# Performance work log

Hardware: AMD Instinct MI355X
Metric: run time of the kernel (lower is better)

Reference implementation:

```python
import jax, jax.numpy as jnp
import numpy as np

D = 512
B = 128
V = 1024
MAX_LEN = 5000


def _pos_encoding(d, max_len):
    # sinusoidal PE table [max_len, d], identical to the torch buffer
    pos = np.arange(max_len, dtype=np.float32)[:, None]
    div = np.exp(np.arange(0, d, 2, dtype=np.float32) * (-np.log(10000.0) / d))
    pe = np.zeros((max_len, d), dtype=np.float32)
    pe[:, 0::2] = np.sin(pos * div)
    pe[:, 1::2] = np.cos(pos * div)
    return jnp.asarray(pe)


def setup_inputs() -> dict:
    key = jax.random.key(0)
    ks = jax.random.split(key, 16)
    s = 0.02  # weight scale
    return {
        "x": jax.random.normal(ks[0], (B, V), jnp.float32),
        "timesteps": jax.random.randint(ks[1], (B,), 0, 1000),
        "query_emb": jax.random.normal(ks[2], (B, D), jnp.float32),
        "target_emb": jax.random.normal(ks[3], (B, V, D), jnp.float32),
        "Wq": jax.random.normal(ks[4], (D, D), jnp.float32) * s,
        "Wk": jax.random.normal(ks[5], (D, D), jnp.float32) * s,
        "Wv": jax.random.normal(ks[6], (D, D), jnp.float32) * s,
        "Wp": jax.random.normal(ks[7], (D, D), jnp.float32) * s,
        "bp": jnp.zeros((D,), jnp.float32),
        "Wt1": jax.random.normal(ks[8], (D, D), jnp.float32) * s,
        "bt1": jnp.zeros((D,), jnp.float32),
        "Wt2": jax.random.normal(ks[9], (D, D), jnp.float32) * s,
        "bt2": jnp.zeros((D,), jnp.float32),
        "Wd1": jax.random.normal(ks[10], (2 * D, 2 * D), jnp.float32) * s,
        "bd1": jnp.zeros((2 * D,), jnp.float32),
        "Wd2": jax.random.normal(ks[11], (1, 2 * D), jnp.float32) * s,
        "bd2": jnp.zeros((1,), jnp.float32),
    }


def reference(x, timesteps, query_emb, target_emb,
              Wq, Wk, Wv, Wp, bp, Wt1, bt1, Wt2, bt2,
              Wd1, bd1, Wd2, bd2):
    pe = _pos_encoding(D, MAX_LEN)
    # timestep embedding: pe[t] -> SiLU MLP  (dropout in eval mode = identity)
    t = pe[timesteps]                                      # [B, D]
    cond = jax.nn.silu(t @ Wt1.T + bt1) @ Wt2.T + bt2      # [B, D]
    q = (query_emb + cond) @ Wq.T                          # [B, D]
    tc = target_emb + cond[:, None, :]                     # [B, V, D]
    k = tc @ Wk.T
    v = tc @ Wv.T
    # single-query attention with additive bias x
    weight = jax.nn.softmax(jnp.einsum('bd,bvd->bv', q, k) + x, axis=-1)  # [B, V]
    new_emb = jnp.einsum('bv,bvd->bd', weight, v) @ Wp.T + bp             # [B, D]
    # concat-MLP decoder over all candidates
    emb = jnp.concatenate(
        [jnp.broadcast_to(new_emb[:, None, :], target_emb.shape), target_emb],
        axis=-1)                                            # [B, V, 2D]
    h = jax.nn.relu(emb @ Wd1.T + bd1)                      # [B, V, 2D]
    p = (h @ Wd2.T + bd2)[..., 0] + weight                  # [B, V]
    return p
```

## Files before the change

kernel.cpp:

```cpp
#include <hip/hip_runtime.h>
#include <hip/hip_bf16.h>


typedef __attribute__((ext_vector_type(8))) short bhalf8_t;
typedef __attribute__((ext_vector_type(8))) unsigned short ushort8_t;
typedef __attribute__((ext_vector_type(4))) float fx4_t;

__device__ __forceinline__ unsigned short f2bf(float f) {
  unsigned int u = __float_as_uint(f);
  unsigned int r = (u + 0x7FFFu + ((u >> 16) & 1u)) >> 16;
  return (unsigned short)r;
}
__device__ __forceinline__ float bf2f(unsigned short h) {
  return __uint_as_float((unsigned int)h << 16);
}

__device__ __forceinline__ float wave_sum64(float s) {
#pragma unroll
  for (int o = 32; o; o >>= 1) s += __shfl_xor(s, o, 64);
  return s;
}

__global__ __launch_bounds__(256) void transpose5_kernel(
    const float* __restrict__ s0, const float* __restrict__ s1, const float* __restrict__ s2,
    const float* __restrict__ s3, const float* __restrict__ s4,
    float* __restrict__ d0, float* __restrict__ d1, float* __restrict__ d2,
    float* __restrict__ d3, float* __restrict__ d4) {
  __shared__ float t[32][33];
  const float* src; float* dst;
  switch (blockIdx.z) {
    case 0: src = s0; dst = d0; break;
    case 1: src = s1; dst = d1; break;
    case 2: src = s2; dst = d2; break;
    case 3: src = s3; dst = d3; break;
    default: src = s4; dst = d4; break;
  }
  const int tx = threadIdx.x & 31, ty = threadIdx.x >> 5;
  const int c0 = blockIdx.x * 32, r0 = blockIdx.y * 32;
#pragma unroll
  for (int i = 0; i < 32; i += 8)
    t[ty + i][tx] = src[(size_t)(r0 + ty + i) * 512 + c0 + tx];
  __syncthreads();
#pragma unroll
  for (int i = 0; i < 32; i += 8)
    dst[(size_t)(c0 + ty + i) * 512 + r0 + tx] = t[tx][ty + i];
}

__global__ __launch_bounds__(256) void transposed1_kernel(const float* __restrict__ src,
                                                          float* __restrict__ dst) {
  __shared__ float t[32][33];
  const int tx = threadIdx.x & 31, ty = threadIdx.x >> 5;
  const int c0 = blockIdx.x * 32, r0 = blockIdx.y * 32;
#pragma unroll
  for (int i = 0; i < 32; i += 8)
    t[ty + i][tx] = src[(size_t)(r0 + ty + i) * 1024 + c0 + tx];
  __syncthreads();
#pragma unroll
  for (int i = 0; i < 32; i += 8)
    dst[(size_t)(c0 + ty + i) * 1024 + r0 + tx] = t[tx][ty + i];
}

template <int MODE, int ACT, int DOT>
__global__ __launch_bounds__(256) void gvec_kernel(
    const float* __restrict__ WT, int n, const float* __restrict__ src1,
    const float* __restrict__ src2, const float* __restrict__ bias,
    const int* __restrict__ timesteps, float* __restrict__ outp,
    float* __restrict__ dotout) {
  __shared__ __attribute__((aligned(16))) float arow[512];
  const int b = blockIdx.x, tid = threadIdx.x;
  if (MODE == 0) {
    const int ts = timesteps[b];
    const float NEG = -9.2103403719761836f / 512.f;
    float dv = expf((float)(2 * tid) * NEG);
    float ang = (float)ts * dv;
    arow[2 * tid] = sinf(ang);
    arow[2 * tid + 1] = cosf(ang);
  } else {
#pragma unroll
    for (int k = tid; k < 512; k += 256) {
      float a;
      if (MODE == 1) {
        a = src1[(size_t)b * 512 + k];
      } else if (MODE == 2) {
        a = src1[(size_t)b * 512 + k] + src2[(size_t)b * 512 + k];
      } else {
        a = src2[(size_t)b * 512 + k];
#pragma unroll
        for (int q = 0; q < 8; ++q) a += src1[((size_t)b * 8 + q) * 512 + k];
      }
      arow[k] = a;
    }
  }
  __syncthreads();
  const int j = blockIdx.y * 256 + tid;
  const float* w = WT + j;
  float s0 = 0.f, s1 = 0.f, s2 = 0.f, s3 = 0.f;
#pragma unroll 4
  for (int k = 0; k < 512; k += 4) {
    s0 = fmaf(arow[k], w[(size_t)k * n], s0);
    s1 = fmaf(arow[k + 1], w[(size_t)(k + 1) * n], s1);
    s2 = fmaf(arow[k + 2], w[(size_t)(k + 2) * n], s2);
    s3 = fmaf(arow[k + 3], w[(size_t)(k + 3) * n], s3);
  }
  float s = (s0 + s1) + (s2 + s3);
  if (bias) s += bias[j];
  if (ACT == 1) s = s / (1.f + expf(-s));
  outp[(size_t)b * n + j] = s;
  if (DOT) {
    float p = s * src2[(size_t)b * 512 + j];
    p = wave_sum64(p);
    __shared__ float rd[4];
    if ((tid & 63) == 0) rd[tid >> 6] = p;
    __syncthreads();
    if (tid == 0) atomicAdd(dotout + b, rd[0] + rd[1] + rd[2] + rd[3]);
  }
}

__global__ __launch_bounds__(256) void convw_kernel(const float* __restrict__ Wd1,
                                                    unsigned short* __restrict__ wsW) {
  const int g = blockIdx.x * 256 + threadIdx.x;
  const int lane = g & 63;
  const int kc = (g >> 6) & 1;
  const int nhn = (g >> 7) & 7;
  const int ks = (g >> 10) & 7;
  const int nc = g >> 13;
  const int j = nc * 128 + (nhn >> 1) * 32 + (nhn & 1) * 16 + (lane & 15);
  const int k = ks * 64 + kc * 32 + (lane >> 4) * 8;
  const float* src = Wd1 + (size_t)j * 1024 + 512 + k;
  float4 f0 = *(const float4*)src;
  float4 f1 = *(const float4*)(src + 4);
  ushort4 h0 = make_ushort4(f2bf(f0.x), f2bf(f0.y), f2bf(f0.z), f2bf(f0.w));
  ushort4 h1 = make_ushort4(f2bf(f1.x), f2bf(f1.y), f2bf(f1.z), f2bf(f1.w));
  ushort4* dst = (ushort4*)((char*)wsW + (size_t)g * 16);
  dst[0] = h0;
  dst[1] = h1;
}

__global__ __launch_bounds__(256) void logits_kernel(
    const float* __restrict__ te, const float* __restrict__ qk,
    const float* __restrict__ constb, const float* __restrict__ x,
    float* __restrict__ logits, unsigned short* __restrict__ te16, int w16) {
  const int wave = threadIdx.x >> 6, lane = threadIdx.x & 63;
  const size_t r = (size_t)blockIdx.x * 4 + wave;
  const int b = (int)(r >> 10);
  const float4* t4 = (const float4*)(te + r * 512);
  const float4* q4 = (const float4*)(qk + (size_t)b * 512);
  float4 a0 = t4[lane], a1 = t4[lane + 64];
  float4 c0 = q4[lane], c1 = q4[lane + 64];
  float s = a0.x * c0.x + a0.y * c0.y + a0.z * c0.z + a0.w * c0.w +
            a1.x * c1.x + a1.y * c1.y + a1.z * c1.z + a1.w * c1.w;
  s = wave_sum64(s);
  if (w16) {
    ushort4 h0 = make_ushort4(f2bf(a0.x), f2bf(a0.y), f2bf(a0.z), f2bf(a0.w));
    ushort4 h1 = make_ushort4(f2bf(a1.x), f2bf(a1.y), f2bf(a1.z), f2bf(a1.w));
    *(ushort4*)(te16 + r * 512 + lane * 4) = h0;
    *(ushort4*)(te16 + r * 512 + 256 + lane * 4) = h1;
  }
  if (lane == 0) logits[r] = s + constb[b] + x[r];
}

__global__ __launch_bounds__(256) void softmax_kernel(
    const float* __restrict__ logits, const float* __restrict__ bd2,
    float* __restrict__ weight, float* __restrict__ out) {
  __shared__ float sm[4];
  const int b = blockIdx.x, tid = threadIdx.x;
  const int wave = tid >> 6, lane = tid & 63;
  float4 l4 = ((const float4*)(logits + (size_t)b * 1024))[tid];
  float m = fmaxf(fmaxf(l4.x, l4.y), fmaxf(l4.z, l4.w));
#pragma unroll
  for (int o = 32; o; o >>= 1) m = fmaxf(m, __shfl_xor(m, o, 64));
  if (lane == 0) sm[wave] = m;
  __syncthreads();
  float M = fmaxf(fmaxf(sm[0], sm[1]), fmaxf(sm[2], sm[3]));
  __syncthreads();
  float e0 = expf(l4.x - M), e1 = expf(l4.y - M), e2 = expf(l4.z - M), e3 = expf(l4.w - M);
  float ssum = wave_sum64(e0 + e1 + e2 + e3);
  if (lane == 0) sm[wave] = ssum;
  __syncthreads();
  float inv = 1.f / (sm[0] + sm[1] + sm[2] + sm[3]);
  float c = bd2[0];
  float4 w4 = make_float4(e0 * inv, e1 * inv, e2 * inv, e3 * inv);
  ((float4*)(weight + (size_t)b * 1024))[tid] = w4;
  ((float4*)(out + (size_t)b * 1024))[tid] = make_float4(w4.x + c, w4.y + c, w4.z + c, w4.w + c);
}

__global__ __launch_bounds__(256) void wsum32_kernel(const float* __restrict__ te,
                                                     const float* __restrict__ weight,
                                                     float* __restrict__ spart) {
  __shared__ float wl[128];
  const int b = blockIdx.x >> 3, vq = blockIdx.x & 7;
  const int tid = threadIdx.x;
  if (tid < 128) wl[tid] = weight[(size_t)b * 1024 + vq * 128 + tid];
  __syncthreads();
  const float* tb = te + ((size_t)b * 1024 + (size_t)vq * 128) * 512;
  float s0 = 0.f, s1 = 0.f;
#pragma unroll 4
  for (int v = 0; v < 128; ++v) {
    float w = wl[v];
    s0 += w * tb[(size_t)v * 512 + tid];
    s1 += w * tb[(size_t)v * 512 + 256 + tid];
  }
  spart[(size_t)blockIdx.x * 512 + tid] = s0;
  spart[(size_t)blockIdx.x * 512 + 256 + tid] = s1;
}

__global__ __launch_bounds__(256) void wsum16_kernel(const unsigned short* __restrict__ te16,
                                                     const float* __restrict__ weight,
                                                     float* __restrict__ spart) {
  __shared__ float wl[128];
  __shared__ float red[4][512];
  const int b = blockIdx.x >> 3, vq = blockIdx.x & 7;
  const int tid = threadIdx.x;
  if (tid < 128) wl[tid] = weight[(size_t)b * 1024 + vq * 128 + tid];
  __syncthreads();
  const int g = tid & 63, vh = tid >> 6;
  const unsigned short* base =
      te16 + ((size_t)b * 1024 + vq * 128 + vh * 32) * 512 + g * 8;
  float acc[8] = {};
  for (int v = 0; v < 32; ++v) {
    float w = wl[vh * 32 + v];
    ushort8_t h = *(const ushort8_t*)(base + (size_t)v * 512);
#pragma unroll
    for (int i = 0; i < 8; ++i) acc[i] += w * bf2f(h[i]);
  }
#pragma unroll
  for (int i = 0; i < 8; ++i) red[vh][g * 8 + i] = acc[i];
  __syncthreads();
  for (int d = tid; d < 512; d += 256)
    spart[(size_t)blockIdx.x * 512 + d] =
        red[0][d] + red[1][d] + red[2][d] + red[3][d];
}

#define GLD16(g, l)                                                              \
  __builtin_amdgcn_global_load_lds((const __attribute__((address_space(1))) void*)(g), \
                                   (__attribute__((address_space(3))) void*)(l), 16, 0, 0)

template <int USE16>
__global__ __launch_bounds__(512, 2) void decoder_kernel(
    const float* __restrict__ te, const unsigned short* __restrict__ te16,
    const unsigned short* __restrict__ wsW, const float* __restrict__ A,
    const float* __restrict__ Wd2, float* __restrict__ out) {
  extern __shared__ char lds[];

  const int tid = threadIdx.x;
  const int wave = tid >> 6, lane = tid & 63;
  const int lhi = lane >> 4, llo = lane & 15;
  const int mh = wave >> 2, nh = wave & 3;
  const size_t row0 = (size_t)blockIdx.x * 64;
  const int b = (int)(blockIdx.x >> 4);

  bhalf8_t a[2][16];
  if (USE16) {
#pragma unroll
    for (int m = 0; m < 2; ++m) {
      const char* rowp = (const char*)te16 + (row0 + mh * 32 + m * 16 + llo) * 1024 + lhi * 16;
#pragma unroll
      for (int s = 0; s < 16; ++s) a[m][s] = *(const bhalf8_t*)(rowp + s * 64);
    }
  } else {
#pragma unroll
    for (int m = 0; m < 2; ++m) {
      const char* rowp = (const char*)te + (row0 + mh * 32 + m * 16 + llo) * 2048 + lhi * 32;
#pragma unroll
      for (int s = 0; s < 16; ++s) {
        float4 f0 = *(const float4*)(rowp + s * 128);
        float4 f1 = *(const float4*)(rowp + s * 128 + 16);
        bhalf8_t h;
        h[0] = (short)f2bf(f0.x); h[1] = (short)f2bf(f0.y);
        h[2] = (short)f2bf(f0.z); h[3] = (short)f2bf(f0.w);
        h[4] = (short)f2bf(f1.x); h[5] = (short)f2bf(f1.y);
        h[6] = (short)f2bf(f1.z); h[7] = (short)f2bf(f1.w);
        a[m][s] = h;
      }
    }
  }

  float av[8][2], wv[8][2];
#pragma unroll
  for (int nc = 0; nc < 8; ++nc) {
    const int jb = nc * 128 + nh * 32 + llo;
    av[nc][0] = A[(size_t)b * 1024 + jb];
    av[nc][1] = A[(size_t)b * 1024 + jb + 16];
    wv[nc][0] = Wd2[jb];
    wv[nc][1] = Wd2[jb + 16];
  }

#pragma unroll
  for (int m = 0; m < 2; ++m)
#pragma unroll
    for (int s = 0; s < 16; ++s) asm volatile("" : "+v"(a[m][s]));
#pragma unroll
  for (int nc = 0; nc < 8; ++nc)
    asm volatile("" : "+v"(av[nc][0]), "+v"(av[nc][1]), "+v"(wv[nc][0]), "+v"(wv[nc][1]));

  auto stage = [&](int c) {
    const char* src = (const char*)wsW + (size_t)c * 16384 + wave * 1024 + lane * 16;
    char* dst = lds + (c & 3) * 16384 + wave * 1024;
    GLD16(src, dst);
    GLD16(src + 8192, dst + 8192);
  };
  stage(0); stage(1); stage(2);

  fx4_t acc[2][2];
  const fx4_t zf = {0.f, 0.f, 0.f, 0.f};
  float pacc[2][4] = {};

#pragma unroll
  for (int nc = 0; nc < 8; ++nc) {
#pragma unroll
    for (int ks = 0; ks < 8; ++ks) {
      const int c = nc * 8 + ks;
      if (c <= 61)      asm volatile("s_waitcnt vmcnt(4)" ::: "memory");
      else if (c == 62) asm volatile("s_waitcnt vmcnt(2)" ::: "memory");
      else              asm volatile("s_waitcnt vmcnt(0)" ::: "memory");
      __builtin_amdgcn_s_barrier();
      __builtin_amdgcn_sched_barrier(0);
      if (ks == 0) { acc[0][0] = zf; acc[0][1] = zf; acc[1][0] = zf; acc[1][1] = zf; }
      const char* wb = lds + (c & 3) * 16384 + nh * 4096 + lane * 16;
      bhalf8_t b00 = *(const bhalf8_t*)(wb);
      bhalf8_t b01 = *(const bhalf8_t*)(wb + 1024);
      bhalf8_t b10 = *(const bhalf8_t*)(wb + 2048);
      bhalf8_t b11 = *(const bhalf8_t*)(wb + 3072);
      acc[0][0] = __builtin_amdgcn_mfma_f32_16x16x32_bf16(a[0][ks * 2 + 0], b00, acc[0][0], 0, 0, 0);
      acc[0][0] = __builtin_amdgcn_mfma_f32_16x16x32_bf16(a[0][ks * 2 + 1], b01, acc[0][0], 0, 0, 0);
      acc[0][1] = __builtin_amdgcn_mfma_f32_16x16x32_bf16(a[0][ks * 2 + 0], b10, acc[0][1], 0, 0, 0);
      acc[0][1] = __builtin_amdgcn_mfma_f32_16x16x32_bf16(a[0][ks * 2 + 1], b11, acc[0][1], 0, 0, 0);
      acc[1][0] = __builtin_amdgcn_mfma_f32_16x16x32_bf16(a[1][ks * 2 + 0], b00, acc[1][0], 0, 0, 0);
      acc[1][0] = __builtin_amdgcn_mfma_f32_16x16x32_bf16(a[1][ks * 2 + 1], b01, acc[1][0], 0, 0, 0);
      acc[1][1] = __builtin_amdgcn_mfma_f32_16x16x32_bf16(a[1][ks * 2 + 0], b10, acc[1][1], 0, 0, 0);
      acc[1][1] = __builtin_amdgcn_mfma_f32_16x16x32_bf16(a[1][ks * 2 + 1], b11, acc[1][1], 0, 0, 0);
      if (c <= 60) stage(c + 3);
      if (ks == 7) {
#pragma unroll
        for (int m = 0; m < 2; ++m)
#pragma unroll
          for (int rg = 0; rg < 4; ++rg)
            pacc[m][rg] += fmaxf(acc[m][0][rg] + av[nc][0], 0.f) * wv[nc][0] +
                           fmaxf(acc[m][1][rg] + av[nc][1], 0.f) * wv[nc][1];
      }
    }
  }

  __syncthreads();
  float* red = (float*)lds;
#pragma unroll
  for (int m = 0; m < 2; ++m)
#pragma unroll
    for (int rg = 0; rg < 4; ++rg) {
      float sv = pacc[m][rg];
      sv += __shfl_xor(sv, 1, 64);
      sv += __shfl_xor(sv, 2, 64);
      sv += __shfl_xor(sv, 4, 64);
      sv += __shfl_xor(sv, 8, 64);
      if (llo == 0) red[nh * 64 + mh * 32 + m * 16 + lhi * 4 + rg] = sv;
    }
  __syncthreads();
  if (tid < 64) {
    float s = red[tid] + red[64 + tid] + red[128 + tid] + red[192 + tid];
    out[row0 + tid] += s;
  }
}

extern "C" void kernel_launch(void* const* d_in, const int* in_sizes, int n_in,
                              void* d_out, int out_size, void* d_ws, size_t ws_size,
                              hipStream_t stream) {
  const float* x = (const float*)d_in[0];
  const int* tsteps = (const int*)d_in[1];
  const float* qe = (const float*)d_in[2];
  const float* te = (const float*)d_in[3];
  const float* Wq = (const float*)d_in[4];
  const float* Wk = (const float*)d_in[5];
  const float* Wv = (const float*)d_in[6];
  const float* Wp = (const float*)d_in[7];
  const float* bp = (const float*)d_in[8];
  const float* Wt1 = (const float*)d_in[9];
  const float* bt1 = (const float*)d_in[10];
  const float* Wt2 = (const float*)d_in[11];
  const float* bt2 = (const float*)d_in[12];
  const float* Wd1 = (const float*)d_in[13];
  const float* bd1 = (const float*)d_in[14];
  const float* Wd2 = (const float*)d_in[15];
  const float* bd2 = (const float*)d_in[16];
  float* out = (float*)d_out;

  char* ws = (char*)d_ws;
  unsigned short* wsW = (unsigned short*)(ws + 0);
  float* Wt1T = (float*)(ws + 1048576);
  float* Wt2T = (float*)(ws + 2097152);
  float* WqT = (float*)(ws + 3145728);
  float* WvT = (float*)(ws + 4194304);
  float* WpT = (float*)(ws + 5242880);
  float* Wd1aT = (float*)(ws + 6291456);
  float* cond = (float*)(ws + 8388608);
  float* qk = (float*)(ws + 8650752);
  float* hbuf = (float*)(ws + 8912896);
  float* qbuf = (float*)(ws + 9175040);
  float* ubuf = (float*)(ws + 9437184);
  float* nebuf = (float*)(ws + 9699328);
  float* cb = (float*)(ws + 9961472);
  float* logits = (float*)(ws + 9965568);
  float* wgt = (float*)(ws + 10489856);
  float* spart = (float*)(ws + 11014144);
  float* Abuf = (float*)(ws + 13111296);
  const size_t TE16_OFF = 14680064;
  const size_t TE16_BYTES = (size_t)128 * 1024 * 512 * 2;
  unsigned short* te16 = (unsigned short*)(ws + TE16_OFF);
  const int use16 = (ws_size >= TE16_OFF + TE16_BYTES) ? 1 : 0;

  transpose5_kernel<<<dim3(16, 16, 5), 256, 0, stream>>>(Wt1, Wt2, Wq, Wv, Wp,
                                                         Wt1T, Wt2T, WqT, WvT, WpT);
  transposed1_kernel<<<dim3(16, 32), 256, 0, stream>>>(Wd1, Wd1aT);
  convw_kernel<<<256, 256, 0, stream>>>(Wd1, wsW);

  hipMemsetAsync(cb, 0, 128 * sizeof(float), stream);
  gvec_kernel<0, 1, 0><<<dim3(128, 2), 256, 0, stream>>>(Wt1T, 512, nullptr, nullptr, bt1, tsteps, hbuf, nullptr);
  gvec_kernel<1, 0, 0><<<dim3(128, 2), 256, 0, stream>>>(Wt2T, 512, hbuf, nullptr, bt2, nullptr, cond, nullptr);
  gvec_kernel<2, 0, 0><<<dim3(128, 2), 256, 0, stream>>>(WqT, 512, qe, cond, nullptr, nullptr, qbuf, nullptr);
  gvec_kernel<1, 0, 1><<<dim3(128, 2), 256, 0, stream>>>(Wk, 512, qbuf, cond, nullptr, nullptr, qk, cb);

  logits_kernel<<<32768, 256, 0, stream>>>(te, qk, cb, x, logits, te16, use16);
  softmax_kernel<<<128, 256, 0, stream>>>(logits, bd2, wgt, out);
  if (use16)
    wsum16_kernel<<<1024, 256, 0, stream>>>(te16, wgt, spart);
  else
    wsum32_kernel<<<1024, 256, 0, stream>>>(te, wgt, spart);

  gvec_kernel<3, 0, 0><<<dim3(128, 2), 256, 0, stream>>>(WvT, 512, spart, cond, nullptr, nullptr, ubuf, nullptr);
  gvec_kernel<1, 0, 0><<<dim3(128, 2), 256, 0, stream>>>(WpT, 512, ubuf, nullptr, bp, nullptr, nebuf, nullptr);
  gvec_kernel<1, 0, 0><<<dim3(128, 4), 256, 0, stream>>>(Wd1aT, 1024, nebuf, nullptr, bd1, nullptr, Abuf, nullptr);

  if (use16) {
    (void)hipFuncSetAttribute((const void*)decoder_kernel<1>,
                              hipFuncAttributeMaxDynamicSharedMemorySize, 65536);
    decoder_kernel<1><<<2048, 512, 65536, stream>>>(te, te16, wsW, Abuf, Wd2, out);
  } else {
    (void)hipFuncSetAttribute((const void*)decoder_kernel<0>,
                              hipFuncAttributeMaxDynamicSharedMemorySize, 65536);
    decoder_kernel<0><<<2048, 512, 65536, stream>>>(te, te16, wsW, Abuf, Wd2, out);
  }
}
```

Before: 474.7 us.

## Restructure decoder GEMM to persistent blocks with LDS-staged activations and register weights

The decoder kernel moves from 2048 blocks, each holding activation rows in registers and streaming Wd1 through LDS, to 256 persistent blocks that each process 8 tiles of 64 rows. Activation tiles are double-buffered in swizzled LDS (async global-to-LDS loads for the bf16 path). Each wave owns 128 output columns and reads its weight fragments directly from global/L2 into registers. The weight pre-layout kernel is re-indexed to match. The aim is more MFMA work per LDS read and fewer per-block barriers. In exchange, the kernel uses about 130KB of LDS and a large accumulator array (one block per CU), and only 256 blocks are launched.

```diff
diff --git a/kernel.cpp b/kernel.cpp
--- a/kernel.cpp
+++ b/kernel.cpp
@@ -120,12 +120,11 @@
                                                     unsigned short* __restrict__ wsW) {
   const int g = blockIdx.x * 256 + threadIdx.x;
   const int lane = g & 63;
-  const int kc = (g >> 6) & 1;
-  const int nhn = (g >> 7) & 7;
-  const int ks = (g >> 10) & 7;
-  const int nc = g >> 13;
-  const int j = nc * 128 + (nhn >> 1) * 32 + (nhn & 1) * 16 + (lane & 15);
-  const int k = ks * 64 + kc * 32 + (lane >> 4) * 8;
+  const int n = (g >> 6) & 7;
+  const int ksw = (g >> 9) & 15;
+  const int nc = (g >> 13) & 7;
+  const int j = nc * 128 + n * 16 + (lane & 15);
+  const int k = ksw * 32 + (lane >> 4) * 8;
   const float* src = Wd1 + (size_t)j * 1024 + 512 + k;
   float4 f0 = *(const float4*)src;
   float4 f1 = *(const float4*)(src + 4);
@@ -245,119 +244,123 @@
   const int tid = threadIdx.x;
   const int wave = tid >> 6, lane = tid & 63;
   const int lhi = lane >> 4, llo = lane & 15;
-  const int mh = wave >> 2, nh = wave & 3;
-  const size_t row0 = (size_t)blockIdx.x * 64;
-  const int b = (int)(blockIdx.x >> 4);
-
-  bhalf8_t a[2][16];
+  const int xr = (llo & 7) << 4;
+  float* red = (float*)(lds + 131072);
+
+  auto stageA16 = [&](int tile) {
+    const char* src = (const char*)te16 + (((size_t)blockIdx.x * 8 + tile) * 64) * 1024;
+    char* dbase = lds + (tile & 1) * 65536;
+#pragma unroll
+    for (int it = 0; it < 8; ++it) {
+      const int r = it * 8 + wave;
+      GLD16(src + r * 1024 + ((lane * 16) ^ (wave << 4)), dbase + r * 1024);
+    }
+  };
+  auto stageA32 = [&](int tile) {
+    const float* src = te + (((size_t)blockIdx.x * 8 + tile) * 64) * 512;
+    char* dbase = lds + (tile & 1) * 65536;
+#pragma unroll
+    for (int it = 0; it < 8; ++it) {
+      int u = it * 512 + tid;
+      int r = u >> 6, c = u & 63;
+      const float4* s = (const float4*)(src + (size_t)r * 512 + c * 8);
+      float4 f0 = s[0], f1 = s[1];
+      ushort4 h0 = make_ushort4(f2bf(f0.x), f2bf(f0.y), f2bf(f0.z), f2bf(f0.w));
+      ushort4 h1 = make_ushort4(f2bf(f1.x), f2bf(f1.y), f2bf(f1.z), f2bf(f1.w));
+      char* d = dbase + r * 1024 + ((c * 16) ^ ((r & 7) << 4));
+      *(ushort4*)d = h0;
+      *(ushort4*)(d + 8) = h1;
+    }
+  };
+
+  auto loadB = [&](bhalf8_t (&dst)[8], int ksw) {
+    const char* p = (const char*)wsW + (((size_t)wave * 16 + ksw) << 13) + lane * 16;
+#pragma unroll
+    for (int n = 0; n < 8; ++n) dst[n] = *(const bhalf8_t*)(p + n * 1024);
+  };
+
+  const int rb0 = llo * 1024;
+  fx4_t acc[4][8];
+  const fx4_t zf = {0.f, 0.f, 0.f, 0.f};
+
   if (USE16) {
-#pragma unroll
-    for (int m = 0; m < 2; ++m) {
-      const char* rowp = (const char*)te16 + (row0 + mh * 32 + m * 16 + llo) * 1024 + lhi * 16;
-#pragma unroll
-      for (int s = 0; s < 16; ++s) a[m][s] = *(const bhalf8_t*)(rowp + s * 64);
-    }
+    stageA16(0);
+    asm volatile("s_waitcnt vmcnt(0)" ::: "memory");
   } else {
-#pragma unroll
-    for (int m = 0; m < 2; ++m) {
-      const char* rowp = (const char*)te + (row0 + mh * 32 + m * 16 + llo) * 2048 + lhi * 32;
-#pragma unroll
-      for (int s = 0; s < 16; ++s) {
-        float4 f0 = *(const float4*)(rowp + s * 128);
-        float4 f1 = *(const float4*)(rowp + s * 128 + 16);
-        bhalf8_t h;
-        h[0] = (short)f2bf(f0.x); h[1] = (short)f2bf(f0.y);
-        h[2] = (short)f2bf(f0.z); h[3] = (short)f2bf(f0.w);
-        h[4] = (short)f2bf(f1.x); h[5] = (short)f2bf(f1.y);
-        h[6] = (short)f2bf(f1.z); h[7] = (short)f2bf(f1.w);
-        a[m][s] = h;
+    stageA32(0);
+  }
+  __syncthreads();
+
+  for (int t = 0; t < 8; ++t) {
+    if (t < 7) {
+      if (USE16) stageA16(t + 1);
+      else       stageA32(t + 1);
+    }
+#pragma unroll
+    for (int m = 0; m < 4; ++m)
+#pragma unroll
+      for (int n = 0; n < 8; ++n) acc[m][n] = zf;
+
+    const char* ab = lds + (t & 1) * 65536;
+    bhalf8_t bA[8], bB[8];
+
+    auto bodyK = [&](bhalf8_t (&bw)[8], int ksw) {
+      const int off = (ksw * 64 + lhi * 16) ^ xr;
+      bhalf8_t a0 = *(const bhalf8_t*)(ab + rb0 + off);
+      bhalf8_t a1 = *(const bhalf8_t*)(ab + rb0 + 16384 + off);
+      bhalf8_t a2 = *(const bhalf8_t*)(ab + rb0 + 32768 + off);
+      bhalf8_t a3 = *(const bhalf8_t*)(ab + rb0 + 49152 + off);
+#pragma unroll
+      for (int n = 0; n < 8; ++n) {
+        acc[0][n] = __builtin_amdgcn_mfma_f32_16x16x32_bf16(a0, bw[n], acc[0][n], 0, 0, 0);
+        acc[1][n] = __builtin_amdgcn_mfma_f32_16x16x32_bf16(a1, bw[n], acc[1][n], 0, 0, 0);
+        acc[2][n] = __builtin_amdgcn_mfma_f32_16x16x32_bf16(a2, bw[n], acc[2][n], 0, 0, 0);
+        acc[3][n] = __builtin_amdgcn_mfma_f32_16x16x32_bf16(a3, bw[n], acc[3][n], 0, 0, 0);
       }
-    }
-  }
-
-  float av[8][2], wv[8][2];
-#pragma unroll
-  for (int nc = 0; nc < 8; ++nc) {
-    const int jb = nc * 128 + nh * 32 + llo;
-    av[nc][0] = A[(size_t)b * 1024 + jb];
-    av[nc][1] = A[(size_t)b * 1024 + jb + 16];
-    wv[nc][0] = Wd2[jb];
-    wv[nc][1] = Wd2[jb + 16];
-  }
-
-#pragma unroll
-  for (int m = 0; m < 2; ++m)
-#pragma unroll
-    for (int s = 0; s < 16; ++s) asm volatile("" : "+v"(a[m][s]));
-#pragma unroll
-  for (int nc = 0; nc < 8; ++nc)
-    asm volatile("" : "+v"(av[nc][0]), "+v"(av[nc][1]), "+v"(wv[nc][0]), "+v"(wv[nc][1]));
-
-  auto stage = [&](int c) {
-    const char* src = (const char*)wsW + (size_t)c * 16384 + wave * 1024 + lane * 16;
-    char* dst = lds + (c & 3) * 16384 + wave * 1024;
-    GLD16(src, dst);
-    GLD16(src + 8192, dst + 8192);
-  };
-  stage(0); stage(1); stage(2);
-
-  fx4_t acc[2][2];
-  const fx4_t zf = {0.f, 0.f, 0.f, 0.f};
-  float pacc[2][4] = {};
-
-#pragma unroll
-  for (int nc = 0; nc < 8; ++nc) {
-#pragma unroll
-    for (int ks = 0; ks < 8; ++ks) {
-      const int c = nc * 8 + ks;
-      if (c <= 61)      asm volatile("s_waitcnt vmcnt(4)" ::: "memory");
-      else if (c == 62) asm volatile("s_waitcnt vmcnt(2)" ::: "memory");
-      else              asm volatile("s_waitcnt vmcnt(0)" ::: "memory");
-      __builtin_amdgcn_s_barrier();
-      __builtin_amdgcn_sched_barrier(0);
-      if (ks == 0) { acc[0][0] = zf; acc[0][1] = zf; acc[1][0] = zf; acc[1][1] = zf; }
-      const char* wb = lds + (c & 3) * 16384 + nh * 4096 + lane * 16;
-      bhalf8_t b00 = *(const bhalf8_t*)(wb);
-      bhalf8_t b01 = *(const bhalf8_t*)(wb + 1024);
-      bhalf8_t b10 = *(const bhalf8_t*)(wb + 2048);
-      bhalf8_t b11 = *(const bhalf8_t*)(wb + 3072);
-      acc[0][0] = __builtin_amdgcn_mfma_f32_16x16x32_bf16(a[0][ks * 2 + 0], b00, acc[0][0], 0, 0, 0);
-      acc[0][0] = __builtin_amdgcn_mfma_f32_16x16x32_bf16(a[0][ks * 2 + 1], b01, acc[0][0], 0, 0, 0);
-      acc[0][1] = __builtin_amdgcn_mfma_f32_16x16x32_bf16(a[0][ks * 2 + 0], b10, acc[0][1], 0, 0, 0);
-      acc[0][1] = __builtin_amdgcn_mfma_f32_16x16x32_bf16(a[0][ks * 2 + 1], b11, acc[0][1], 0, 0, 0);
-      acc[1][0] = __builtin_amdgcn_mfma_f32_16x16x32_bf16(a[1][ks * 2 + 0], b00, acc[1][0], 0, 0, 0);
-      acc[1][0] = __builtin_amdgcn_mfma_f32_16x16x32_bf16(a[1][ks * 2 + 1], b01, acc[1][0], 0, 0, 0);
-      acc[1][1] = __builtin_amdgcn_mfma_f32_16x16x32_bf16(a[1][ks * 2 + 0], b10, acc[1][1], 0, 0, 0);
-      acc[1][1] = __builtin_amdgcn_mfma_f32_16x16x32_bf16(a[1][ks * 2 + 1], b11, acc[1][1], 0, 0, 0);
-      if (c <= 60) stage(c + 3);
-      if (ks == 7) {
-#pragma unroll
-        for (int m = 0; m < 2; ++m)
-#pragma unroll
-          for (int rg = 0; rg < 4; ++rg)
-            pacc[m][rg] += fmaxf(acc[m][0][rg] + av[nc][0], 0.f) * wv[nc][0] +
-                           fmaxf(acc[m][1][rg] + av[nc][1], 0.f) * wv[nc][1];
+    };
+
+    loadB(bA, 0);
+#pragma unroll
+    for (int kp = 0; kp < 8; ++kp) {
+      loadB(bB, 2 * kp + 1);
+      bodyK(bA, 2 * kp);
+      if (kp < 7) loadB(bA, 2 * kp + 2);
+      bodyK(bB, 2 * kp + 1);
+    }
+
+    const int tg = (int)blockIdx.x * 8 + t;
+    const float* A_g = A + (size_t)(tg >> 4) * 1024;
+    float pacc[4][4] = {};
+#pragma unroll
+    for (int n = 0; n < 8; ++n) {
+      const int j = wave * 128 + n * 16 + llo;
+      const float av = A_g[j];
+      const float wvv = Wd2[j];
+#pragma unroll
+      for (int m = 0; m < 4; ++m)
+#pragma unroll
+        for (int rg = 0; rg < 4; ++rg)
+          pacc[m][rg] += fmaxf(acc[m][n][rg] + av, 0.f) * wvv;
+    }
+    __syncthreads();
+#pragma unroll
+    for (int m = 0; m < 4; ++m)
+#pragma unroll
+      for (int rg = 0; rg < 4; ++rg) {
+        float sv = pacc[m][rg];
+        sv += __shfl_xor(sv, 1, 64);
+        sv += __shfl_xor(sv, 2, 64);
+        sv += __shfl_xor(sv, 4, 64);
+        sv += __shfl_xor(sv, 8, 64);
+        if (llo == 0) red[wave * 64 + m * 16 + lhi * 4 + rg] = sv;
       }
-    }
-  }
-
-  __syncthreads();
-  float* red = (float*)lds;
-#pragma unroll
-  for (int m = 0; m < 2; ++m)
-#pragma unroll
-    for (int rg = 0; rg < 4; ++rg) {
-      float sv = pacc[m][rg];
-      sv += __shfl_xor(sv, 1, 64);
-      sv += __shfl_xor(sv, 2, 64);
-      sv += __shfl_xor(sv, 4, 64);
-      sv += __shfl_xor(sv, 8, 64);
-      if (llo == 0) red[nh * 64 + mh * 32 + m * 16 + lhi * 4 + rg] = sv;
-    }
-  __syncthreads();
-  if (tid < 64) {
-    float s = red[tid] + red[64 + tid] + red[128 + tid] + red[192 + tid];
-    out[row0 + tid] += s;
+    __syncthreads();
+    if (tid < 64) {
+      float s = 0.f;
+#pragma unroll
+      for (int w = 0; w < 8; ++w) s += red[w * 64 + tid];
+      out[(size_t)tg * 64 + tid] += s;
+    }
   }
 }
 
@@ -431,11 +434,11 @@
 
   if (use16) {
     (void)hipFuncSetAttribute((const void*)decoder_kernel<1>,
-                              hipFuncAttributeMaxDynamicSharedMemorySize, 65536);
-    decoder_kernel<1><<<2048, 512, 65536, stream>>>(te, te16, wsW, Abuf, Wd2, out);
+                              hipFuncAttributeMaxDynamicSharedMemorySize, 133120);
+    decoder_kernel<1><<<256, 512, 133120, stream>>>(te, te16, wsW, Abuf, Wd2, out);
   } else {
     (void)hipFuncSetAttribute((const void*)decoder_kernel<0>,
-                              hipFuncAttributeMaxDynamicSharedMemorySize, 65536);
-    decoder_kernel<0><<<2048, 512, 65536, stream>>>(te, te16, wsW, Abuf, Wd2, out);
-  }
-}
+                              hipFuncAttributeMaxDynamicSharedMemorySize, 133120);
+    decoder_kernel<0><<<256, 512, 133120, stream>>>(te, te16, wsW, Abuf, Wd2, out);
+  }
+}
```

New measurement: 758.9 us. 1.6x slower.

## Stage decoder A-tile in swizzled LDS instead of registers

Applied to the files above, without the earlier changes.

The decoder kernel no longer holds its 64x512 bf16 target-embedding tile in VGPRs. It loads the tile into an XOR-swizzled region of LDS, via direct global-to-LDS loads in the bf16 path, and reads A fragments from LDS on each k-step. The bias and Wd2 values are also loaded lazily in the epilogue rather than kept in registers. This cuts register pressure, which could allow more waves or better scheduling, but it doubles dynamic LDS to 128 KB per block, which likely limits residency to one block per CU, and it adds LDS read traffic inside the MFMA loop.

```diff
diff --git a/kernel.cpp b/kernel.cpp
--- a/kernel.cpp
+++ b/kernel.cpp
@@ -241,6 +241,7 @@
     const unsigned short* __restrict__ wsW, const float* __restrict__ A,
     const float* __restrict__ Wd2, float* __restrict__ out) {
   extern __shared__ char lds[];
+  char* ring = lds + 65536;
 
   const int tid = threadIdx.x;
   const int wave = tid >> 6, lane = tid & 63;
@@ -249,58 +250,49 @@
   const size_t row0 = (size_t)blockIdx.x * 64;
   const int b = (int)(blockIdx.x >> 4);
 
-  bhalf8_t a[2][16];
-  if (USE16) {
-#pragma unroll
-    for (int m = 0; m < 2; ++m) {
-      const char* rowp = (const char*)te16 + (row0 + mh * 32 + m * 16 + llo) * 1024 + lhi * 16;
-#pragma unroll
-      for (int s = 0; s < 16; ++s) a[m][s] = *(const bhalf8_t*)(rowp + s * 64);
-    }
-  } else {
-#pragma unroll
-    for (int m = 0; m < 2; ++m) {
-      const char* rowp = (const char*)te + (row0 + mh * 32 + m * 16 + llo) * 2048 + lhi * 32;
-#pragma unroll
-      for (int s = 0; s < 16; ++s) {
-        float4 f0 = *(const float4*)(rowp + s * 128);
-        float4 f1 = *(const float4*)(rowp + s * 128 + 16);
-        bhalf8_t h;
-        h[0] = (short)f2bf(f0.x); h[1] = (short)f2bf(f0.y);
-        h[2] = (short)f2bf(f0.z); h[3] = (short)f2bf(f0.w);
-        h[4] = (short)f2bf(f1.x); h[5] = (short)f2bf(f1.y);
-        h[6] = (short)f2bf(f1.z); h[7] = (short)f2bf(f1.w);
-        a[m][s] = h;
-      }
-    }
-  }
-
-  float av[8][2], wv[8][2];
-#pragma unroll
-  for (int nc = 0; nc < 8; ++nc) {
-    const int jb = nc * 128 + nh * 32 + llo;
-    av[nc][0] = A[(size_t)b * 1024 + jb];
-    av[nc][1] = A[(size_t)b * 1024 + jb + 16];
-    wv[nc][0] = Wd2[jb];
-    wv[nc][1] = Wd2[jb + 16];
-  }
-
-#pragma unroll
-  for (int m = 0; m < 2; ++m)
-#pragma unroll
-    for (int s = 0; s < 16; ++s) asm volatile("" : "+v"(a[m][s]));
-#pragma unroll
-  for (int nc = 0; nc < 8; ++nc)
-    asm volatile("" : "+v"(av[nc][0]), "+v"(av[nc][1]), "+v"(wv[nc][0]), "+v"(wv[nc][1]));
-
   auto stage = [&](int c) {
     const char* src = (const char*)wsW + (size_t)c * 16384 + wave * 1024 + lane * 16;
-    char* dst = lds + (c & 3) * 16384 + wave * 1024;
+    char* dst = ring + (c & 3) * 16384 + wave * 1024;
     GLD16(src, dst);
     GLD16(src + 8192, dst + 8192);
   };
-  stage(0); stage(1); stage(2);
-
+
+  if (USE16) {
+    const char* src = (const char*)te16 + row0 * 1024;
+#pragma unroll
+    for (int it = 0; it < 8; ++it) {
+      const int r = it * 8 + wave;
+      GLD16(src + (size_t)r * 1024 + ((lane * 16) ^ (wave << 4)), lds + r * 1024);
+    }
+    stage(0); stage(1); stage(2);
+    asm volatile("s_waitcnt vmcnt(6)" ::: "memory");
+  } else {
+    const float* src = te + row0 * 512;
+#pragma unroll
+    for (int it = 0; it < 8; ++it) {
+      int u = it * 512 + tid;
+      int r = u >> 6, c = u & 63;
+      const float4* s = (const float4*)(src + (size_t)r * 512 + c * 8);
+      float4 f0 = s[0], f1 = s[1];
+      ushort4 h0 = make_ushort4(f2bf(f0.x), f2bf(f0.y), f2bf(f0.z), f2bf(f0.w));
+      ushort4 h1 = make_ushort4(f2bf(f1.x), f2bf(f1.y), f2bf(f1.z), f2bf(f1.w));
+      char* d = lds + r * 1024 + ((c * 16) ^ ((r & 7) << 4));
+      *(ushort4*)d = h0;
+      *(ushort4*)(d + 8) = h1;
+    }
+    stage(0); stage(1); stage(2);
+  }
+  __syncthreads();
+
+  int aoffb[2][2];
+#pragma unroll
+  for (int m = 0; m < 2; ++m)
+#pragma unroll
+    for (int kc = 0; kc < 2; ++kc)
+      aoffb[m][kc] = (mh * 32 + m * 16 + llo) * 1024 +
+                     ((kc * 64 + lhi * 16) ^ ((llo & 7) << 4));
+
+  const float* A_g = A + (size_t)b * 1024;
   fx4_t acc[2][2];
   const fx4_t zf = {0.f, 0.f, 0.f, 0.f};
   float pacc[2][4] = {};
@@ -316,33 +308,43 @@
       __builtin_amdgcn_s_barrier();
       __builtin_amdgcn_sched_barrier(0);
       if (ks == 0) { acc[0][0] = zf; acc[0][1] = zf; acc[1][0] = zf; acc[1][1] = zf; }
-      const char* wb = lds + (c & 3) * 16384 + nh * 4096 + lane * 16;
+      const char* wb = ring + (c & 3) * 16384 + nh * 4096 + lane * 16;
+      const char* tb = lds + ks * 128;
+      bhalf8_t a00 = *(const bhalf8_t*)(tb + aoffb[0][0]);
+      bhalf8_t a01 = *(const bhalf8_t*)(tb + aoffb[0][1]);
+      bhalf8_t a10 = *(const bhalf8_t*)(tb + aoffb[1][0]);
+      bhalf8_t a11 = *(const bhalf8_t*)(tb + aoffb[1][1]);
       bhalf8_t b00 = *(const bhalf8_t*)(wb);
       bhalf8_t b01 = *(const bhalf8_t*)(wb + 1024);
       bhalf8_t b10 = *(const bhalf8_t*)(wb + 2048);
       bhalf8_t b11 = *(const bhalf8_t*)(wb + 3072);
-      acc[0][0] = __builtin_amdgcn_mfma_f32_16x16x32_bf16(a[0][ks * 2 + 0], b00, acc[0][0], 0, 0, 0);
-      acc[0][0] = __builtin_amdgcn_mfma_f32_16x16x32_bf16(a[0][ks * 2 + 1], b01, acc[0][0], 0, 0, 0);
-      acc[0][1] = __builtin_amdgcn_mfma_f32_16x16x32_bf16(a[0][ks * 2 + 0], b10, acc[0][1], 0, 0, 0);
-      acc[0][1] = __builtin_amdgcn_mfma_f32_16x16x32_bf16(a[0][ks * 2 + 1], b11, acc[0][1], 0, 0, 0);
-      acc[1][0] = __builtin_amdgcn_mfma_f32_16x16x32_bf16(a[1][ks * 2 + 0], b00, acc[1][0], 0, 0, 0);
-      acc[1][0] = __builtin_amdgcn_mfma_f32_16x16x32_bf16(a[1][ks * 2 + 1], b01, acc[1][0], 0, 0, 0);
-      acc[1][1] = __builtin_amdgcn_mfma_f32_16x16x32_bf16(a[1][ks * 2 + 0], b10, acc[1][1], 0, 0, 0);
-      acc[1][1] = __builtin_amdgcn_mfma_f32_16x16x32_bf16(a[1][ks * 2 + 1], b11, acc[1][1], 0, 0, 0);
+      acc[0][0] = __builtin_amdgcn_mfma_f32_16x16x32_bf16(a00, b00, acc[0][0], 0, 0, 0);
+      acc[0][0] = __builtin_amdgcn_mfma_f32_16x16x32_bf16(a01, b01, acc[0][0], 0, 0, 0);
+      acc[0][1] = __builtin_amdgcn_mfma_f32_16x16x32_bf16(a00, b10, acc[0][1], 0, 0, 0);
+      acc[0][1] = __builtin_amdgcn_mfma_f32_16x16x32_bf16(a01, b11, acc[0][1], 0, 0, 0);
+      acc[1][0] = __builtin_amdgcn_mfma_f32_16x16x32_bf16(a10, b00, acc[1][0], 0, 0, 0);
+      acc[1][0] = __builtin_amdgcn_mfma_f32_16x16x32_bf16(a11, b01, acc[1][0], 0, 0, 0);
+      acc[1][1] = __builtin_amdgcn_mfma_f32_16x16x32_bf16(a10, b10, acc[1][1], 0, 0, 0);
+      acc[1][1] = __builtin_amdgcn_mfma_f32_16x16x32_bf16(a11, b11, acc[1][1], 0, 0, 0);
       if (c <= 60) stage(c + 3);
       if (ks == 7) {
 #pragma unroll
-        for (int m = 0; m < 2; ++m)
-#pragma unroll
-          for (int rg = 0; rg < 4; ++rg)
-            pacc[m][rg] += fmaxf(acc[m][0][rg] + av[nc][0], 0.f) * wv[nc][0] +
-                           fmaxf(acc[m][1][rg] + av[nc][1], 0.f) * wv[nc][1];
+        for (int n = 0; n < 2; ++n) {
+          const int j = nc * 128 + nh * 32 + n * 16 + llo;
+          const float av = A_g[j];
+          const float wvv = Wd2[j];
+#pragma unroll
+          for (int m = 0; m < 2; ++m)
+#pragma unroll
+            for (int rg = 0; rg < 4; ++rg)
+              pacc[m][rg] += fmaxf(acc[m][n][rg] + av, 0.f) * wvv;
+        }
       }
     }
   }
 
   __syncthreads();
-  float* red = (float*)lds;
+  float* red = (float*)ring;
 #pragma unroll
   for (int m = 0; m < 2; ++m)
 #pragma unroll
@@ -431,11 +433,11 @@
 
   if (use16) {
     (void)hipFuncSetAttribute((const void*)decoder_kernel<1>,
-                              hipFuncAttributeMaxDynamicSharedMemorySize, 65536);
-    decoder_kernel<1><<<2048, 512, 65536, stream>>>(te, te16, wsW, Abuf, Wd2, out);
+                              hipFuncAttributeMaxDynamicSharedMemorySize, 131072);
+    decoder_kernel<1><<<2048, 512, 131072, stream>>>(te, te16, wsW, Abuf, Wd2, out);
   } else {
     (void)hipFuncSetAttribute((const void*)decoder_kernel<0>,
-                              hipFuncAttributeMaxDynamicSharedMemorySize, 65536);
-    decoder_kernel<0><<<2048, 512, 65536, stream>>>(te, te16, wsW, Abuf, Wd2, out);
-  }
-}
+                              hipFuncAttributeMaxDynamicSharedMemorySize, 131072);
+    decoder_kernel<0><<<2048, 512, 131072, stream>>>(te, te16, wsW, Abuf, Wd2, out);
+  }
+}
```

New measurement: 410.5 us. 13.5% less time.
